# Kernel optimization log

Measured on AMD Instinct MI355X. Metric: run time of the kernel, lower is better.

## Reference

```python
import jax, jax.numpy as jnp
import numpy as np

D_STATE = 16
D_CONV = 4
TOKEN = 8
GROUPS = 4
EPS = 1e-5


def _gn(x, w, b):
    # GroupNorm(GROUPS) over [B,C,H,W]
    B, C, H, W = x.shape
    xr = x.reshape(B, GROUPS, C // GROUPS, H * W)
    mu = xr.mean((2, 3), keepdims=True)
    var = xr.var((2, 3), keepdims=True)
    xn = ((xr - mu) * jax.lax.rsqrt(var + EPS)).reshape(B, C, H, W)
    return xn * w[None, :, None, None] + b[None, :, None, None]


def _mamba(x, in_w, conv_w, conv_b, xp_w, dt_w, dt_b, A_log, Dp, out_w, dt_rank):
    # mamba_ssm Mamba forward: x [B, L, d_model]
    Bn, L, _ = x.shape
    d_inner = conv_w.shape[0]
    xz = jnp.einsum('bld,ed->ble', x, in_w)          # [B,L,2*d_inner]
    xc, z = jnp.split(xz, 2, axis=-1)
    # causal depthwise conv1d (pad left d_conv-1)
    xt = jnp.pad(jnp.transpose(xc, (0, 2, 1)), ((0, 0), (0, 0), (D_CONV - 1, 0)))
    xt = jax.lax.conv_general_dilated(xt, conv_w[:, None, :], (1,), 'VALID',
                                      dimension_numbers=('NCH', 'OIH', 'NCH'),
                                      feature_group_count=d_inner)
    xc = jax.nn.silu(jnp.transpose(xt, (0, 2, 1)) + conv_b)
    dbl = jnp.einsum('ble,fe->blf', xc, xp_w)        # [B,L,dt_rank+2*d_state]
    dt = dbl[..., :dt_rank]
    Bm = dbl[..., dt_rank:dt_rank + D_STATE]
    Cm = dbl[..., dt_rank + D_STATE:]
    delta = jax.nn.softplus(jnp.einsum('blr,er->ble', dt, dt_w) + dt_b)
    A = -jnp.exp(A_log)                              # [d_inner, d_state]

    def step(h, inp):
        u_t, d_t, b_t, c_t = inp                     # [B,d_inner],[B,d_inner],[B,d_state],[B,d_state]
        dA = jnp.exp(d_t[..., None] * A)
        h = h * dA + (d_t * u_t)[..., None] * b_t[:, None, :]
        return h, jnp.sum(h * c_t[:, None, :], axis=-1)

    xs = (jnp.transpose(xc, (1, 0, 2)), jnp.transpose(delta, (1, 0, 2)),
          jnp.transpose(Bm, (1, 0, 2)), jnp.transpose(Cm, (1, 0, 2)))
    h0 = jnp.zeros((Bn, d_inner, D_STATE), x.dtype)
    _, ys = jax.lax.scan(step, h0, xs)
    y = (jnp.transpose(ys, (1, 0, 2)) + xc * Dp) * jax.nn.silu(z)
    return jnp.einsum('ble,de->bld', y, out_w)


def _mamba_params(key, d_model, dt_rank):
    d_inner = 2 * d_model
    ks = jax.random.split(key, 5)
    p = {}
    p['in_w'] = jax.random.normal(ks[0], (2 * d_inner, d_model)) / np.sqrt(d_model).astype(np.float32)
    p['conv_w'] = jax.random.normal(ks[1], (d_inner, D_CONV)) * 0.3
    p['conv_b'] = jnp.zeros((d_inner,))
    p['xp_w'] = jax.random.normal(ks[2], (dt_rank + 2 * D_STATE, d_inner)) / np.sqrt(d_inner).astype(np.float32)
    p['dt_w'] = jax.random.normal(ks[3], (d_inner, dt_rank)) / np.sqrt(dt_rank).astype(np.float32)
    p['dt_b'] = jnp.full((d_inner,), float(np.log(np.expm1(0.01))))
    p['A_log'] = jnp.log(jnp.broadcast_to(jnp.arange(1, D_STATE + 1, dtype=jnp.float32), (d_inner, D_STATE)))
    p['D'] = jnp.ones((d_inner,))
    p['out_w'] = jax.random.normal(ks[4], (d_model, d_inner)) / np.sqrt(d_inner).astype(np.float32)
    return p


def setup_inputs() -> dict:
    key = jax.random.key(0)
    k1, k2, k3 = jax.random.split(key, 3)
    B, C, H, W = 2, 64, 128, 128
    inp = {'x': jax.random.normal(k1, (B, C, H, W), dtype=jnp.float32)}
    spa = _mamba_params(k2, C, 4)
    spe = _mamba_params(k3, C // TOKEN, 1)
    for n, p in (('spa', spa), ('spe', spe)):
        for k, v in p.items():
            inp[f'{n}_{k}'] = v
    inp['spa_gn_w'] = jnp.ones((C,)); inp['spa_gn_b'] = jnp.zeros((C,))
    inp['spe_gn_w'] = jnp.ones((C,)); inp['spe_gn_b'] = jnp.zeros((C,))
    inp['fuse_w'] = jnp.full((2,), 0.5)
    return inp


def reference(x, spa_in_w, spa_conv_w, spa_conv_b, spa_xp_w, spa_dt_w, spa_dt_b,
              spa_A_log, spa_D, spa_out_w, spe_in_w, spe_conv_w, spe_conv_b,
              spe_xp_w, spe_dt_w, spe_dt_b, spe_A_log, spe_D, spe_out_w,
              spa_gn_w, spa_gn_b, spe_gn_w, spe_gn_b, fuse_w):
    B, C, H, W = x.shape
    # SpaMamba: scan over flattened spatial sequence
    xs = jnp.transpose(x, (0, 2, 3, 1)).reshape(B, H * W, C)
    ys = _mamba(xs, spa_in_w, spa_conv_w, spa_conv_b, spa_xp_w, spa_dt_w, spa_dt_b,
                spa_A_log, spa_D, spa_out_w, 4)
    spa = jnp.transpose(ys.reshape(B, H, W, C), (0, 3, 1, 2))
    spa = jax.nn.silu(_gn(spa, spa_gn_w, spa_gn_b)) + x
    # SpeMamba: scan over channel tokens per pixel (C == TOKEN * gc, no padding)
    gc = C // TOKEN
    xe = jnp.transpose(x, (0, 2, 3, 1)).reshape(B * H * W, TOKEN, gc)
    ye = _mamba(xe, spe_in_w, spe_conv_w, spe_conv_b, spe_xp_w, spe_dt_w, spe_dt_b,
                spe_A_log, spe_D, spe_out_w, 1)
    spe = jnp.transpose(ye.reshape(B, H, W, C), (0, 3, 1, 2))
    spe = jax.nn.silu(_gn(spe, spe_gn_w, spe_gn_b)) + x
    w = jax.nn.softmax(fuse_w)
    return spa * w[0] + spe * w[1] + x
```

## Files before the change

kernel.cpp:

```cpp
#include <hip/hip_runtime.h>
#include <math.h>


#define NB 2
#define NC 64
#define HW_ 16384
#define SCH 512
#define SLC 32

__device__ __forceinline__ float sigmoidf_(float v) { return 1.f / (1.f + __expf(-v)); }
__device__ __forceinline__ float siluf_(float v)    { return v * sigmoidf_(v); }
__device__ __forceinline__ float softplusf_(float v) {
    return v > 0.f ? v + log1pf(__expf(-v)) : log1pf(__expf(v));
}

#define K1_XS_OFF 8576
#define K1_XS_STR 68
#define K1_XCL_STR 132

__global__ __launch_bounds__(256) void k1_spatial_pre(
    const float* __restrict__ x, const float* __restrict__ in_w,
    const float* __restrict__ conv_w, const float* __restrict__ conv_b,
    const float* __restrict__ xp_w, const float* __restrict__ dt_w,
    const float* __restrict__ dt_b, const float* __restrict__ A_log,
    float* __restrict__ xc_g, float* __restrict__ sz_g,
    float* __restrict__ dtp_g, float* __restrict__ Bm_g, float* __restrict__ Cm_g,
    float* __restrict__ cumA_g, float* __restrict__ hsum_g)
{
    __shared__ __align__(16) float smem[13132];
    __shared__ __align__(16) float sB[64 * 16];
    __shared__ __align__(16) float sdt[64 * 4];
    const int tid = threadIdx.x;
    const int b   = blockIdx.x >> 8;
    const int l0  = (blockIdx.x & 255) << 6;

    for (int i = tid; i < 67 * 64; i += 256) {
        int c = i / 67;
        int tok = i - c * 67;
        int l = l0 + tok - 3;
        float v = (l >= 0) ? x[((size_t)b * NC + c) * HW_ + l] : 0.f;
        smem[K1_XS_OFF + tok * K1_XS_STR + c] = v;
    }
    __syncthreads();

    {
        const int e = tid & 127;
        const int half = tid >> 7;
        float w[64];
        #pragma unroll
        for (int q = 0; q < 16; ++q) {
            float4 wv = *(const float4*)(in_w + e * 64 + q * 4);
            w[q*4] = wv.x; w[q*4+1] = wv.y; w[q*4+2] = wv.z; w[q*4+3] = wv.w;
        }
        int t0 = half ? 34 : 0, t1 = half ? 67 : 34;
        for (int tok = t0; tok < t1; ++tok) {
            const float4* xr = (const float4*)(smem + K1_XS_OFF + tok * K1_XS_STR);
            float acc = 0.f;
            #pragma unroll
            for (int q = 0; q < 16; ++q) {
                float4 xv = xr[q];
                acc += w[q*4]*xv.x + w[q*4+1]*xv.y + w[q*4+2]*xv.z + w[q*4+3]*xv.w;
            }
            smem[tok * 128 + e] = acc;
        }
        #pragma unroll
        for (int q = 0; q < 16; ++q) {
            float4 wv = *(const float4*)(in_w + (128 + e) * 64 + q * 4);
            w[q*4] = wv.x; w[q*4+1] = wv.y; w[q*4+2] = wv.z; w[q*4+3] = wv.w;
        }
        int z0 = half * 32;
        for (int tok = z0; tok < z0 + 32; ++tok) {
            const float4* xr = (const float4*)(smem + K1_XS_OFF + (tok + 3) * K1_XS_STR);
            float acc = 0.f;
            #pragma unroll
            for (int q = 0; q < 16; ++q) {
                float4 xv = xr[q];
                acc += w[q*4]*xv.x + w[q*4+1]*xv.y + w[q*4+2]*xv.z + w[q*4+3]*xv.w;
            }
            sz_g[((size_t)(b * HW_ + l0 + tok)) * 128 + e] = siluf_(acc);
        }
    }
    __syncthreads();

    {
        const int e = tid & 127;
        float cw0 = conv_w[e*4], cw1 = conv_w[e*4+1], cw2 = conv_w[e*4+2], cw3 = conv_w[e*4+3];
        float cb = conv_b[e];
        float r[32];
        #pragma unroll
        for (int k = 0; k < 32; ++k) {
            int tok = (tid + k * 256) >> 7;
            float v = cb + cw0 * smem[(tok+0)*128 + e] + cw1 * smem[(tok+1)*128 + e]
                         + cw2 * smem[(tok+2)*128 + e] + cw3 * smem[(tok+3)*128 + e];
            v = siluf_(v);
            r[k] = v;
            xc_g[((size_t)(b * HW_ + l0 + tok)) * 128 + e] = v;
        }
        __syncthreads();
        #pragma unroll
        for (int k = 0; k < 32; ++k) {
            int tok = (tid + k * 256) >> 7;
            smem[tok * K1_XCL_STR + e] = r[k];
        }
    }
    __syncthreads();

    for (int i = tid; i < 64 * 32; i += 256) {
        int tok = i >> 5;
        int f = i & 31;
        const float4* xr = (const float4*)(smem + tok * K1_XCL_STR);
        const float4* wr = (const float4*)(xp_w + (4 + f) * 128);
        float acc = 0.f;
        #pragma unroll
        for (int q = 0; q < 32; ++q) {
            float4 a = xr[q], w4 = wr[q];
            acc += a.x*w4.x + a.y*w4.y + a.z*w4.z + a.w*w4.w;
        }
        size_t row = (size_t)(b * HW_ + l0 + tok);
        if (f < 16) { Bm_g[row * 16 + f] = acc; sB[tok * 16 + f] = acc; }
        else        Cm_g[row * 16 + (f - 16)] = acc;
    }
    {
        int tok = tid >> 2;
        const float4* xr = (const float4*)(smem + tok * K1_XCL_STR);
        const float4* wr = (const float4*)(xp_w + (tid & 3) * 128);
        float acc = 0.f;
        #pragma unroll
        for (int q = 0; q < 32; ++q) {
            float4 a = xr[q], w4 = wr[q];
            acc += a.x*w4.x + a.y*w4.y + a.z*w4.z + a.w*w4.w;
        }
        dtp_g[(size_t)(b * HW_ + l0) * 4 + tid] = acc;
        sdt[tid] = acc;
    }
    __syncthreads();

    {
        const int e = tid >> 1;
        const int n0 = (tid & 1) * 8;
        float A[8];
        #pragma unroll
        for (int j = 0; j < 8; ++j) A[j] = -__expf(A_log[e * 16 + n0 + j]);
        float4 wdt = *(const float4*)(dt_w + e * 4);
        float dtb = dt_b[e];
        #pragma unroll 1
        for (int cc = 0; cc < 2; ++cc) {
            float h[8], cA[8];
            #pragma unroll
            for (int j = 0; j < 8; ++j) { h[j] = 0.f; cA[j] = 1.f; }
            for (int t = cc * 32; t < cc * 32 + 32; ++t) {
                float4 dv = *(const float4*)(sdt + t * 4);
                float d = softplusf_(wdt.x*dv.x + wdt.y*dv.y + wdt.z*dv.z + wdt.w*dv.w + dtb);
                float u = smem[t * K1_XCL_STR + e];
                float4 b0 = *(const float4*)(sB + t * 16 + n0);
                float4 b1 = *(const float4*)(sB + t * 16 + n0 + 4);
                float Bv[8]; *(float4*)(Bv) = b0; *(float4*)(Bv + 4) = b1;
                float du = d * u;
                #pragma unroll
                for (int j = 0; j < 8; ++j) {
                    float dA = __expf(d * A[j]);
                    h[j] = h[j] * dA + du * Bv[j];
                    cA[j] *= dA;
                }
            }
            int ch = ((blockIdx.x & 255) << 1) + cc;
            size_t so = ((size_t)b * SCH + ch) * 2048 + tid * 8;
            *(float4*)(cumA_g + so)     = *(float4*)(cA);
            *(float4*)(cumA_g + so + 4) = *(float4*)(cA + 4);
            *(float4*)(hsum_g + so)     = *(float4*)(h);
            *(float4*)(hsum_g + so + 4) = *(float4*)(h + 4);
        }
    }
}

__global__ __launch_bounds__(256) void k3_combine(
    const float* __restrict__ cumA_g, const float* __restrict__ hsum_g,
    float* __restrict__ Hin_g)
{
    int gid = blockIdx.x * 256 + threadIdx.x;
    int b = gid >> 11;
    int en = gid & 2047;
    float st = 0.f;
    size_t o = (size_t)b * SCH * 2048 + en;
    for (int cb = 0; cb < SCH; cb += 16) {
        float a[16], hs[16];
        #pragma unroll
        for (int k = 0; k < 16; ++k) {
            a[k]  = cumA_g[o + (size_t)k * 2048];
            hs[k] = hsum_g[o + (size_t)k * 2048];
        }
        #pragma unroll
        for (int k = 0; k < 16; ++k) {
            Hin_g[o + (size_t)k * 2048] = st;
            st = st * a[k] + hs[k];
        }
        o += (size_t)16 * 2048;
    }
}

__global__ __launch_bounds__(256) void k4_scan2(
    const float* __restrict__ xc_g, const float* __restrict__ sz_g,
    const float* __restrict__ Bm_g, const float* __restrict__ Cm_g,
    const float* __restrict__ dtp_g, const float* __restrict__ dt_w,
    const float* __restrict__ dt_b, const float* __restrict__ A_log,
    const float* __restrict__ Dp, const float* __restrict__ Hin_g,
    const float* __restrict__ out_w,
    float* __restrict__ spa_raw, float* __restrict__ part_spa)
{
    __shared__ __align__(16) float lds[9344];
    float* su  = lds;
    float* sB  = lds + 4096;
    float* sC  = lds + 4608;
    float* sdt = lds + 5120;
    float* yt  = lds + 5248;
    float* ot  = lds;
    __shared__ float wred[32];
    const int tid = threadIdx.x;
    const int b = blockIdx.x >> 9;
    const int ch = blockIdx.x & 511;
    const size_t rowbase = (size_t)b * HW_ + ch * SLC;

    const float4* u4 = (const float4*)(xc_g + rowbase * 128);
    #pragma unroll
    for (int j = 0; j < 4; ++j) ((float4*)su)[tid + j * 256] = u4[tid + j * 256];
    if (tid < 128) ((float4*)sB)[tid] = ((const float4*)(Bm_g + rowbase * 16))[tid];
    else           ((float4*)sC)[tid - 128] = ((const float4*)(Cm_g + rowbase * 16))[tid - 128];
    if (tid < 32)  ((float4*)sdt)[tid] = ((const float4*)(dtp_g + rowbase * 4))[tid];

    const int e = tid >> 1;
    const int nh = tid & 1;
    const int n0 = nh * 8;
    float A[8];
    #pragma unroll
    for (int j = 0; j < 8; ++j) A[j] = -__expf(A_log[e * 16 + n0 + j]);
    float4 wdt = *(const float4*)(dt_w + e * 4);
    float dtb = dt_b[e];
    float Dv = Dp[e];
    float h[8];
    size_t so = (size_t)blockIdx.x * 2048 + tid * 8;
    *(float4*)(h)     = *(const float4*)(Hin_g + so);
    *(float4*)(h + 4) = *(const float4*)(Hin_g + so + 4);
    __syncthreads();

    for (int t = 0; t < SLC; ++t) {
        float4 dv = *(const float4*)(sdt + t * 4);
        float d = softplusf_(wdt.x*dv.x + wdt.y*dv.y + wdt.z*dv.z + wdt.w*dv.w + dtb);
        float u = su[t * 128 + e];
        float4 b0 = *(const float4*)(sB + t * 16 + n0);
        float4 b1 = *(const float4*)(sB + t * 16 + n0 + 4);
        float4 c0 = *(const float4*)(sC + t * 16 + n0);
        float4 c1 = *(const float4*)(sC + t * 16 + n0 + 4);
        float Bv[8]; *(float4*)(Bv) = b0; *(float4*)(Bv + 4) = b1;
        float Cv[8]; *(float4*)(Cv) = c0; *(float4*)(Cv + 4) = c1;
        float du = d * u;
        float y = 0.f;
        #pragma unroll
        for (int j = 0; j < 8; ++j) {
            float dA = __expf(d * A[j]);
            h[j] = h[j] * dA + du * Bv[j];
            y += h[j] * Cv[j];
        }
        y += __shfl_xor(y, 1, 64);
        if (nh == 0) yt[t * 128 + e] = y + u * Dv;
    }
    __syncthreads();

    {
        const float4* sz4 = (const float4*)(sz_g + rowbase * 128);
        #pragma unroll
        for (int j = 0; j < 4; ++j) {
            int f = tid + j * 256;
            float4 yv = ((float4*)yt)[f];
            float4 sv = sz4[f];
            yv.x *= sv.x; yv.y *= sv.y; yv.z *= sv.z; yv.w *= sv.w;
            ((float4*)yt)[f] = yv;
        }
    }
    __syncthreads();

    for (int i = tid; i < 64 * SLC; i += 256) {
        int c = i & 63, t = i >> 6;
        const float4* wr = (const float4*)(out_w + c * 128);
        const float4* yr = (const float4*)(yt + t * 128);
        float acc = 0.f;
        #pragma unroll
        for (int q = 0; q < 32; ++q) {
            float4 w4 = wr[q], yv4 = yr[q];
            acc += w4.x*yv4.x + w4.y*yv4.y + w4.z*yv4.z + w4.w*yv4.w;
        }
        ot[c * 33 + t] = acc;
    }
    __syncthreads();

    for (int i = tid; i < 64 * SLC; i += 256) {
        int c = i >> 5, t = i & 31;
        spa_raw[((size_t)b * NC + c) * HW_ + ch * SLC + t] = ot[c * 33 + t];
    }
    float s[4], s2[4];
    #pragma unroll
    for (int g = 0; g < 4; ++g) {
        float a = 0.f, a2 = 0.f;
        for (int i = tid; i < 512; i += 256) {
            int c = 16 * g + (i >> 5), t = i & 31;
            float v = ot[c * 33 + t];
            a += v; a2 += v * v;
        }
        s[g] = a; s2[g] = a2;
    }
    #pragma unroll
    for (int g = 0; g < 4; ++g) {
        #pragma unroll
        for (int o = 1; o < 64; o <<= 1) {
            s[g]  += __shfl_xor(s[g], o, 64);
            s2[g] += __shfl_xor(s2[g], o, 64);
        }
    }
    if ((tid & 63) == 0) {
        int w = tid >> 6;
        #pragma unroll
        for (int g = 0; g < 4; ++g) { wred[w*8 + g*2] = s[g]; wred[w*8 + g*2 + 1] = s2[g]; }
    }
    __syncthreads();
    if (tid < 8)
        part_spa[tid * 1024 + blockIdx.x] = wred[tid] + wred[8+tid] + wred[16+tid] + wred[24+tid];
}

__global__ __launch_bounds__(256) void k5_spectral(
    const float* __restrict__ x, const float* __restrict__ in_w,
    const float* __restrict__ conv_w, const float* __restrict__ conv_b,
    const float* __restrict__ xp_w, const float* __restrict__ dt_w,
    const float* __restrict__ dt_b, const float* __restrict__ A_log,
    const float* __restrict__ Dp, const float* __restrict__ out_w,
    float* __restrict__ spe_raw, float* __restrict__ part_spe)
{
    __shared__ float xin[16 * 65];
    __shared__ float sBw[16 * 17];
    __shared__ float sCw[16 * 17];
    __shared__ float ys[16 * 136];
    __shared__ float outs[64 * 17];
    __shared__ float wred[32];
    const int tid = threadIdx.x;
    const int b = blockIdx.x >> 10;
    const int hw0 = (blockIdx.x & 1023) << 4;
    const int s = tid >> 4;
    const int l = tid & 15;
    const int base = tid & 48;

    for (int i = tid; i < 1024; i += 256) {
        int c = i >> 4, j = i & 15;
        xin[j * 65 + c] = x[((size_t)b * NC + c) * HW_ + hw0 + j];
    }
    {
        int l2 = tid >> 4, e2 = tid & 15;
        sBw[l2 * 17 + e2] = xp_w[(1 + l2) * 16 + e2];
        sCw[l2 * 17 + e2] = xp_w[(17 + l2) * 16 + e2];
    }

    float wdt[16];
    #pragma unroll
    for (int e = 0; e < 16; ++e) wdt[e] = xp_w[e];
    float wi0[8], wi1[8];
    #pragma unroll
    for (int c = 0; c < 8; ++c) { wi0[c] = in_w[l*8 + c]; wi1[c] = in_w[(l+16)*8 + c]; }
    float cw0 = conv_w[l*4], cw1 = conv_w[l*4+1], cw2 = conv_w[l*4+2], cw3 = conv_w[l*4+3];
    float cb = conv_b[l];
    float dtw = dt_w[l], dtb = dt_b[l];
    __syncthreads();

    float pre[8], sz[8];
    #pragma unroll
    for (int t = 0; t < 8; ++t) {
        float a0 = 0.f, a1 = 0.f;
        #pragma unroll
        for (int c = 0; c < 8; ++c) {
            float xv = xin[s * 65 + t * 8 + c];
            a0 += wi0[c] * xv; a1 += wi1[c] * xv;
        }
        pre[t] = a0; sz[t] = siluf_(a1);
    }
    float xcv[8];
    #pragma unroll
    for (int t = 0; t < 8; ++t) {
        float v = cb + cw3 * pre[t];
        if (t >= 1) v += cw2 * pre[t-1];
        if (t >= 2) v += cw1 * pre[t-2];
        if (t >= 3) v += cw0 * pre[t-3];
        xcv[t] = siluf_(v);
    }

    float bn[8], cn[8], dd0[8];
    #pragma unroll
    for (int t = 0; t < 8; ++t) { bn[t] = 0.f; cn[t] = 0.f; dd0[t] = 0.f; }
    #pragma unroll
    for (int e = 0; e < 16; ++e) {
        float wBe = sBw[l * 17 + e];
        float wCe = sCw[l * 17 + e];
        float wde = wdt[e];
        #pragma unroll
        for (int t = 0; t < 8; ++t) {
            float xv = __shfl(xcv[t], base + e, 64);
            bn[t] += wBe * xv; cn[t] += wCe * xv; dd0[t] += wde * xv;
        }
    }
    float del[8];
    #pragma unroll
    for (int t = 0; t < 8; ++t) del[t] = softplusf_(dd0[t] * dtw + dtb);

    float A[16];
    #pragma unroll
    for (int n = 0; n < 16; ++n) A[n] = -__expf(A_log[l * 16 + n]);
    float Dv = Dp[l];
    float h[16];
    #pragma unroll
    for (int n = 0; n < 16; ++n) h[n] = 0.f;
    #pragma unroll
    for (int t = 0; t < 8; ++t) {
        float d = del[t], u = xcv[t];
        float du = d * u;
        float y = 0.f;
        #pragma unroll
        for (int n = 0; n < 16; ++n) {
            float Bn = __shfl(bn[t], base + n, 64);
            float Cn = __shfl(cn[t], base + n, 64);
            float dA = __expf(d * A[n]);
            h[n] = h[n] * dA + du * Bn;
            y += h[n] * Cn;
        }
        ys[s * 136 + t * 17 + l] = (y + u * Dv) * sz[t];
    }
    __syncthreads();

    {
        int t = l >> 1;
        int db = (l & 1) * 4;
        #pragma unroll
        for (int jj = 0; jj < 4; ++jj) {
            int dd = db + jj;
            float acc = 0.f;
            #pragma unroll
            for (int e = 0; e < 16; ++e) acc += out_w[dd * 16 + e] * ys[s * 136 + t * 17 + e];
            outs[(t * 8 + dd) * 17 + s] = acc;
        }
    }
    __syncthreads();

    float sg[4], sg2[4];
    #pragma unroll
    for (int k = 0; k < 4; ++k) {
        int i = tid + k * 256;
        int c = i >> 4, j = i & 15;
        float v = outs[c * 17 + j];
        spe_raw[((size_t)b * NC + c) * HW_ + hw0 + j] = v;
        sg[k] = v; sg2[k] = v * v;
    }
    #pragma unroll
    for (int k = 0; k < 4; ++k) {
        #pragma unroll
        for (int o = 1; o < 64; o <<= 1) {
            sg[k]  += __shfl_xor(sg[k], o, 64);
            sg2[k] += __shfl_xor(sg2[k], o, 64);
        }
    }
    if ((tid & 63) == 0) {
        int w = tid >> 6;
        #pragma unroll
        for (int k = 0; k < 4; ++k) { wred[w*8 + k*2] = sg[k]; wred[w*8 + k*2 + 1] = sg2[k]; }
    }
    __syncthreads();
    if (tid < 8)
        part_spe[tid * 2048 + blockIdx.x] = wred[tid] + wred[8+tid] + wred[16+tid] + wred[24+tid];
}

__global__ __launch_bounds__(256) void k5b_stats(
    const float* __restrict__ part_spa, const float* __restrict__ part_spe,
    float* __restrict__ stats)
{
    __shared__ float fina[16], fine_[16];
    const int tid = threadIdx.x;
    const int combo = tid >> 4;
    const int ln = tid & 15;
    const int slot = combo & 7, bb = combo >> 3;
    {
        const float4* p = (const float4*)(part_spa + slot * 1024 + bb * 512);
        float a = 0.f;
        #pragma unroll
        for (int k = 0; k < 8; ++k) {
            float4 v = p[ln * 8 + k];
            a += v.x + v.y + v.z + v.w;
        }
        #pragma unroll
        for (int o = 1; o < 16; o <<= 1) a += __shfl_xor(a, o, 64);
        if (ln == 0) fina[combo] = a;
    }
    {
        const float4* p = (const float4*)(part_spe + slot * 2048 + bb * 1024);
        float a = 0.f;
        #pragma unroll
        for (int k = 0; k < 16; ++k) {
            float4 v = p[ln * 16 + k];
            a += v.x + v.y + v.z + v.w;
        }
        #pragma unroll
        for (int o = 1; o < 16; o <<= 1) a += __shfl_xor(a, o, 64);
        if (ln == 0) fine_[combo] = a;
    }
    __syncthreads();
    if (tid < 16) {
        int branch = tid >> 3, bb2 = (tid >> 2) & 1, g = tid & 3;
        const float* fin = branch ? fine_ : fina;
        float S  = fin[bb2 * 8 + g * 2];
        float S2 = fin[bb2 * 8 + g * 2 + 1];
        const float N = 262144.f;
        float mu = S / N;
        float var = S2 / N - mu * mu;
        stats[tid * 2] = mu;
        stats[tid * 2 + 1] = rsqrtf(var + 1e-5f);
    }
}

__global__ __launch_bounds__(256) void k6_fuse(
    const float* __restrict__ x, const float* __restrict__ spa_raw,
    const float* __restrict__ spe_raw, const float* __restrict__ stats,
    const float* __restrict__ gwa, const float* __restrict__ gba,
    const float* __restrict__ gwe, const float* __restrict__ gbe,
    const float* __restrict__ fw, float* __restrict__ out)
{
    size_t i4 = (size_t)blockIdx.x * 256 + threadIdx.x;
    size_t base = i4 * 4;
    int b = (int)(base >> 20);
    int rem = (int)(base & 1048575);
    int c = rem >> 14;
    int g = c >> 4;
    int sidx = (b * 4 + g) * 2;
    float ma = stats[sidx],      ra = stats[sidx + 1];
    float me = stats[16 + sidx], re = stats[16 + sidx + 1];
    float wa = gwa[c], ba = gba[c], we = gwe[c], be = gbe[c];
    float f0 = fw[0], f1 = fw[1];
    float mx = fmaxf(f0, f1);
    float e0 = __expf(f0 - mx), e1 = __expf(f1 - mx);
    float inv = 1.f / (e0 + e1);
    float w0 = e0 * inv, w1 = e1 * inv;
    float4 xv = *(const float4*)(x + base);
    float4 av = *(const float4*)(spa_raw + base);
    float4 ev = *(const float4*)(spe_raw + base);
    float xr[4] = {xv.x, xv.y, xv.z, xv.w};
    float ar[4] = {av.x, av.y, av.z, av.w};
    float er[4] = {ev.x, ev.y, ev.z, ev.w};
    float orr[4];
    #pragma unroll
    for (int k = 0; k < 4; ++k) {
        float spa = siluf_((ar[k] - ma) * ra * wa + ba) + xr[k];
        float spe = siluf_((er[k] - me) * re * we + be) + xr[k];
        orr[k] = spa * w0 + spe * w1 + xr[k];
    }
    float4 ov = {orr[0], orr[1], orr[2], orr[3]};
    *(float4*)(out + base) = ov;
}

extern "C" void kernel_launch(void* const* d_in, const int* in_sizes, int n_in,
                              void* d_out, int out_size, void* d_ws, size_t ws_size,
                              hipStream_t stream)
{
    const float* x      = (const float*)d_in[0];
    const float* a_inw  = (const float*)d_in[1];
    const float* a_cw   = (const float*)d_in[2];
    const float* a_cb   = (const float*)d_in[3];
    const float* a_xp   = (const float*)d_in[4];
    const float* a_dtw  = (const float*)d_in[5];
    const float* a_dtb  = (const float*)d_in[6];
    const float* a_Alog = (const float*)d_in[7];
    const float* a_D    = (const float*)d_in[8];
    const float* a_ow   = (const float*)d_in[9];
    const float* e_inw  = (const float*)d_in[10];
    const float* e_cw   = (const float*)d_in[11];
    const float* e_cb   = (const float*)d_in[12];
    const float* e_xp   = (const float*)d_in[13];
    const float* e_dtw  = (const float*)d_in[14];
    const float* e_dtb  = (const float*)d_in[15];
    const float* e_Alog = (const float*)d_in[16];
    const float* e_D    = (const float*)d_in[17];
    const float* e_ow   = (const float*)d_in[18];
    const float* gwa    = (const float*)d_in[19];
    const float* gba    = (const float*)d_in[20];
    const float* gwe    = (const float*)d_in[21];
    const float* gbe    = (const float*)d_in[22];
    const float* fw     = (const float*)d_in[23];

    float* ws    = (float*)d_ws;
    float* xc    = ws;
    float* sz    = xc    + 4194304;
    float* Bm    = sz    + 4194304;
    float* Cm    = Bm    + 524288;
    float* dtp   = Cm    + 524288;
    float* cumA  = dtp   + 131072;
    float* hsum  = cumA  + 2097152;
    float* Hin   = hsum  + 2097152;
    float* spa_r = Hin   + 2097152;
    float* spe_r = spa_r + 2097152;
    float* pspa  = spe_r + 2097152;
    float* pspe  = pspa  + 8192;
    float* stats = pspe  + 16384;

    k1_spatial_pre<<<512, 256, 0, stream>>>(x, a_inw, a_cw, a_cb, a_xp, a_dtw,
                                            a_dtb, a_Alog,
                                            xc, sz, dtp, Bm, Cm, cumA, hsum);
    k3_combine<<<16, 256, 0, stream>>>(cumA, hsum, Hin);
    k5_spectral<<<2048, 256, 0, stream>>>(x, e_inw, e_cw, e_cb, e_xp, e_dtw, e_dtb,
                                          e_Alog, e_D, e_ow, spe_r, pspe);
    k4_scan2<<<1024, 256, 0, stream>>>(xc, sz, Bm, Cm, dtp, a_dtw, a_dtb, a_Alog,
                                       a_D, Hin, a_ow, spa_r, pspa);
    k5b_stats<<<1, 256, 0, stream>>>(pspa, pspe, stats);
    k6_fuse<<<2048, 256, 0, stream>>>(x, spa_r, spe_r, stats, gwa, gba, gwe, gbe, fw,
                                      (float*)d_out);
}
```

Before: 413.6 us.

## Halve spatial pre-kernel tile and restage spectral B/C projections through LDS

```diff
diff --git a/kernel.cpp b/kernel.cpp
--- a/kernel.cpp
+++ b/kernel.cpp
@@ -14,7 +14,7 @@
     return v > 0.f ? v + log1pf(__expf(-v)) : log1pf(__expf(v));
 }
 
-#define K1_XS_OFF 8576
+#define K1_XS_OFF 4480
 #define K1_XS_STR 68
 #define K1_XCL_STR 132
 
@@ -27,16 +27,16 @@
     float* __restrict__ dtp_g, float* __restrict__ Bm_g, float* __restrict__ Cm_g,
     float* __restrict__ cumA_g, float* __restrict__ hsum_g)
 {
-    __shared__ __align__(16) float smem[13132];
-    __shared__ __align__(16) float sB[64 * 16];
-    __shared__ __align__(16) float sdt[64 * 4];
+    __shared__ __align__(16) float smem[6860];
+    __shared__ __align__(16) float sB[32 * 16];
+    __shared__ __align__(16) float sdt[32 * 4];
     const int tid = threadIdx.x;
-    const int b   = blockIdx.x >> 8;
-    const int l0  = (blockIdx.x & 255) << 6;
-
-    for (int i = tid; i < 67 * 64; i += 256) {
-        int c = i / 67;
-        int tok = i - c * 67;
+    const int b   = blockIdx.x >> 9;
+    const int l0  = (blockIdx.x & 511) << 5;
+
+    for (int i = tid; i < 35 * 64; i += 256) {
+        int c = i / 35;
+        int tok = i - c * 35;
         int l = l0 + tok - 3;
         float v = (l >= 0) ? x[((size_t)b * NC + c) * HW_ + l] : 0.f;
         smem[K1_XS_OFF + tok * K1_XS_STR + c] = v;
@@ -52,7 +52,7 @@
             float4 wv = *(const float4*)(in_w + e * 64 + q * 4);
             w[q*4] = wv.x; w[q*4+1] = wv.y; w[q*4+2] = wv.z; w[q*4+3] = wv.w;
         }
-        int t0 = half ? 34 : 0, t1 = half ? 67 : 34;
+        int t0 = half ? 18 : 0, t1 = half ? 35 : 18;
         for (int tok = t0; tok < t1; ++tok) {
             const float4* xr = (const float4*)(smem + K1_XS_OFF + tok * K1_XS_STR);
             float acc = 0.f;
@@ -68,8 +68,8 @@
             float4 wv = *(const float4*)(in_w + (128 + e) * 64 + q * 4);
             w[q*4] = wv.x; w[q*4+1] = wv.y; w[q*4+2] = wv.z; w[q*4+3] = wv.w;
         }
-        int z0 = half * 32;
-        for (int tok = z0; tok < z0 + 32; ++tok) {
+        int z0 = half * 16;
+        for (int tok = z0; tok < z0 + 16; ++tok) {
             const float4* xr = (const float4*)(smem + K1_XS_OFF + (tok + 3) * K1_XS_STR);
             float acc = 0.f;
             #pragma unroll
@@ -86,9 +86,9 @@
         const int e = tid & 127;
         float cw0 = conv_w[e*4], cw1 = conv_w[e*4+1], cw2 = conv_w[e*4+2], cw3 = conv_w[e*4+3];
         float cb = conv_b[e];
-        float r[32];
-        #pragma unroll
-        for (int k = 0; k < 32; ++k) {
+        float r[16];
+        #pragma unroll
+        for (int k = 0; k < 16; ++k) {
             int tok = (tid + k * 256) >> 7;
             float v = cb + cw0 * smem[(tok+0)*128 + e] + cw1 * smem[(tok+1)*128 + e]
                          + cw2 * smem[(tok+2)*128 + e] + cw3 * smem[(tok+3)*128 + e];
@@ -98,14 +98,14 @@
         }
         __syncthreads();
         #pragma unroll
-        for (int k = 0; k < 32; ++k) {
+        for (int k = 0; k < 16; ++k) {
             int tok = (tid + k * 256) >> 7;
             smem[tok * K1_XCL_STR + e] = r[k];
         }
     }
     __syncthreads();
 
-    for (int i = tid; i < 64 * 32; i += 256) {
+    for (int i = tid; i < 32 * 32; i += 256) {
         int tok = i >> 5;
         int f = i & 31;
         const float4* xr = (const float4*)(smem + tok * K1_XCL_STR);
@@ -120,7 +120,7 @@
         if (f < 16) { Bm_g[row * 16 + f] = acc; sB[tok * 16 + f] = acc; }
         else        Cm_g[row * 16 + (f - 16)] = acc;
     }
-    {
+    if (tid < 128) {
         int tok = tid >> 2;
         const float4* xr = (const float4*)(smem + tok * K1_XCL_STR);
         const float4* wr = (const float4*)(xp_w + (tid & 3) * 128);
@@ -143,33 +143,29 @@
         for (int j = 0; j < 8; ++j) A[j] = -__expf(A_log[e * 16 + n0 + j]);
         float4 wdt = *(const float4*)(dt_w + e * 4);
         float dtb = dt_b[e];
-        #pragma unroll 1
-        for (int cc = 0; cc < 2; ++cc) {
-            float h[8], cA[8];
+        float h[8], cA[8];
+        #pragma unroll
+        for (int j = 0; j < 8; ++j) { h[j] = 0.f; cA[j] = 1.f; }
+        for (int t = 0; t < 32; ++t) {
+            float4 dv = *(const float4*)(sdt + t * 4);
+            float d = softplusf_(wdt.x*dv.x + wdt.y*dv.y + wdt.z*dv.z + wdt.w*dv.w + dtb);
+            float u = smem[t * K1_XCL_STR + e];
+            float4 b0 = *(const float4*)(sB + t * 16 + n0);
+            float4 b1 = *(const float4*)(sB + t * 16 + n0 + 4);
+            float Bv[8]; *(float4*)(Bv) = b0; *(float4*)(Bv + 4) = b1;
+            float du = d * u;
             #pragma unroll
-            for (int j = 0; j < 8; ++j) { h[j] = 0.f; cA[j] = 1.f; }
-            for (int t = cc * 32; t < cc * 32 + 32; ++t) {
-                float4 dv = *(const float4*)(sdt + t * 4);
-                float d = softplusf_(wdt.x*dv.x + wdt.y*dv.y + wdt.z*dv.z + wdt.w*dv.w + dtb);
-                float u = smem[t * K1_XCL_STR + e];
-                float4 b0 = *(const float4*)(sB + t * 16 + n0);
-                float4 b1 = *(const float4*)(sB + t * 16 + n0 + 4);
-                float Bv[8]; *(float4*)(Bv) = b0; *(float4*)(Bv + 4) = b1;
-                float du = d * u;
-                #pragma unroll
-                for (int j = 0; j < 8; ++j) {
-                    float dA = __expf(d * A[j]);
-                    h[j] = h[j] * dA + du * Bv[j];
-                    cA[j] *= dA;
-                }
+            for (int j = 0; j < 8; ++j) {
+                float dA = __expf(d * A[j]);
+                h[j] = h[j] * dA + du * Bv[j];
+                cA[j] *= dA;
             }
-            int ch = ((blockIdx.x & 255) << 1) + cc;
-            size_t so = ((size_t)b * SCH + ch) * 2048 + tid * 8;
-            *(float4*)(cumA_g + so)     = *(float4*)(cA);
-            *(float4*)(cumA_g + so + 4) = *(float4*)(cA + 4);
-            *(float4*)(hsum_g + so)     = *(float4*)(h);
-            *(float4*)(hsum_g + so + 4) = *(float4*)(h + 4);
-        }
+        }
+        size_t so = (size_t)blockIdx.x * 2048 + tid * 8;
+        *(float4*)(cumA_g + so)     = *(float4*)(cA);
+        *(float4*)(cumA_g + so + 4) = *(float4*)(cA + 4);
+        *(float4*)(hsum_g + so)     = *(float4*)(h);
+        *(float4*)(hsum_g + so + 4) = *(float4*)(h + 4);
     }
 }
 
@@ -325,7 +321,9 @@
         part_spa[tid * 1024 + blockIdx.x] = wred[tid] + wred[8+tid] + wred[16+tid] + wred[24+tid];
 }
 
-__global__ __launch_bounds__(256) void k5_spectral(
+#define K5_STR 144
+
+__global__ __launch_bounds__(256, 2) void k5_spectral(
     const float* __restrict__ x, const float* __restrict__ in_w,
     const float* __restrict__ conv_w, const float* __restrict__ conv_b,
     const float* __restrict__ xp_w, const float* __restrict__ dt_w,
@@ -333,49 +331,50 @@
     const float* __restrict__ Dp, const float* __restrict__ out_w,
     float* __restrict__ spe_raw, float* __restrict__ part_spe)
 {
-    __shared__ float xin[16 * 65];
-    __shared__ float sBw[16 * 17];
-    __shared__ float sCw[16 * 17];
-    __shared__ float ys[16 * 136];
-    __shared__ float outs[64 * 17];
+    __shared__ __align__(16) float lds[7936];
+    float* xcs  = lds;
+    float* sBn  = lds + 2304;
+    float* sCn  = lds + 4608;
+    float* souw = lds + 6912;
+    float* xin  = sBn;
+    float* ys   = xcs;
+    float* outs = sCn;
     __shared__ float wred[32];
     const int tid = threadIdx.x;
     const int b = blockIdx.x >> 10;
     const int hw0 = (blockIdx.x & 1023) << 4;
     const int s = tid >> 4;
     const int l = tid & 15;
-    const int base = tid & 48;
 
     for (int i = tid; i < 1024; i += 256) {
         int c = i >> 4, j = i & 15;
-        xin[j * 65 + c] = x[((size_t)b * NC + c) * HW_ + hw0 + j];
-    }
-    {
-        int l2 = tid >> 4, e2 = tid & 15;
-        sBw[l2 * 17 + e2] = xp_w[(1 + l2) * 16 + e2];
-        sCw[l2 * 17 + e2] = xp_w[(17 + l2) * 16 + e2];
-    }
-
-    float wdt[16];
-    #pragma unroll
-    for (int e = 0; e < 16; ++e) wdt[e] = xp_w[e];
+        xin[j * 68 + c] = x[((size_t)b * NC + c) * HW_ + hw0 + j];
+        souw[i] = out_w[i];
+    }
     float wi0[8], wi1[8];
     #pragma unroll
     for (int c = 0; c < 8; ++c) { wi0[c] = in_w[l*8 + c]; wi1[c] = in_w[(l+16)*8 + c]; }
     float cw0 = conv_w[l*4], cw1 = conv_w[l*4+1], cw2 = conv_w[l*4+2], cw3 = conv_w[l*4+3];
     float cb = conv_b[l];
     float dtw = dt_w[l], dtb = dt_b[l];
+    float wdt[16], wB[16], wC[16];
+    #pragma unroll
+    for (int e = 0; e < 16; ++e) {
+        wdt[e] = xp_w[e];
+        wB[e]  = xp_w[(1 + l) * 16 + e];
+        wC[e]  = xp_w[(17 + l) * 16 + e];
+    }
     __syncthreads();
 
     float pre[8], sz[8];
     #pragma unroll
     for (int t = 0; t < 8; ++t) {
-        float a0 = 0.f, a1 = 0.f;
-        #pragma unroll
-        for (int c = 0; c < 8; ++c) {
-            float xv = xin[s * 65 + t * 8 + c];
-            a0 += wi0[c] * xv; a1 += wi1[c] * xv;
-        }
+        float4 x0 = *(const float4*)(xin + s * 68 + t * 8);
+        float4 x1 = *(const float4*)(xin + s * 68 + t * 8 + 4);
+        float a0 = wi0[0]*x0.x + wi0[1]*x0.y + wi0[2]*x0.z + wi0[3]*x0.w
+                 + wi0[4]*x1.x + wi0[5]*x1.y + wi0[6]*x1.z + wi0[7]*x1.w;
+        float a1 = wi1[0]*x0.x + wi1[1]*x0.y + wi1[2]*x0.z + wi1[3]*x0.w
+                 + wi1[4]*x1.x + wi1[5]*x1.y + wi1[6]*x1.z + wi1[7]*x1.w;
         pre[t] = a0; sz[t] = siluf_(a1);
     }
     float xcv[8];
@@ -387,24 +386,32 @@
         if (t >= 3) v += cw0 * pre[t-3];
         xcv[t] = siluf_(v);
     }
-
-    float bn[8], cn[8], dd0[8];
-    #pragma unroll
-    for (int t = 0; t < 8; ++t) { bn[t] = 0.f; cn[t] = 0.f; dd0[t] = 0.f; }
-    #pragma unroll
-    for (int e = 0; e < 16; ++e) {
-        float wBe = sBw[l * 17 + e];
-        float wCe = sCw[l * 17 + e];
-        float wde = wdt[e];
-        #pragma unroll
-        for (int t = 0; t < 8; ++t) {
-            float xv = __shfl(xcv[t], base + e, 64);
-            bn[t] += wBe * xv; cn[t] += wCe * xv; dd0[t] += wde * xv;
-        }
-    }
+    #pragma unroll
+    for (int t = 0; t < 8; ++t) xcs[s * K5_STR + t * 16 + l] = xcv[t];
+    __syncthreads();
+
     float del[8];
     #pragma unroll
-    for (int t = 0; t < 8; ++t) del[t] = softplusf_(dd0[t] * dtw + dtb);
+    for (int t = 0; t < 8; ++t) {
+        const float4* xr = (const float4*)(xcs + s * K5_STR + t * 16);
+        float4 v0 = xr[0], v1 = xr[1], v2 = xr[2], v3 = xr[3];
+        float bn = wB[0]*v0.x + wB[1]*v0.y + wB[2]*v0.z + wB[3]*v0.w
+                 + wB[4]*v1.x + wB[5]*v1.y + wB[6]*v1.z + wB[7]*v1.w
+                 + wB[8]*v2.x + wB[9]*v2.y + wB[10]*v2.z + wB[11]*v2.w
+                 + wB[12]*v3.x + wB[13]*v3.y + wB[14]*v3.z + wB[15]*v3.w;
+        float cn = wC[0]*v0.x + wC[1]*v0.y + wC[2]*v0.z + wC[3]*v0.w
+                 + wC[4]*v1.x + wC[5]*v1.y + wC[6]*v1.z + wC[7]*v1.w
+                 + wC[8]*v2.x + wC[9]*v2.y + wC[10]*v2.z + wC[11]*v2.w
+                 + wC[12]*v3.x + wC[13]*v3.y + wC[14]*v3.z + wC[15]*v3.w;
+        float d0 = wdt[0]*v0.x + wdt[1]*v0.y + wdt[2]*v0.z + wdt[3]*v0.w
+                 + wdt[4]*v1.x + wdt[5]*v1.y + wdt[6]*v1.z + wdt[7]*v1.w
+                 + wdt[8]*v2.x + wdt[9]*v2.y + wdt[10]*v2.z + wdt[11]*v2.w
+                 + wdt[12]*v3.x + wdt[13]*v3.y + wdt[14]*v3.z + wdt[15]*v3.w;
+        sBn[s * K5_STR + t * 16 + l] = bn;
+        sCn[s * K5_STR + t * 16 + l] = cn;
+        del[t] = softplusf_(d0 * dtw + dtb);
+    }
+    __syncthreads();
 
     float A[16];
     #pragma unroll
@@ -418,27 +425,35 @@
         float d = del[t], u = xcv[t];
         float du = d * u;
         float y = 0.f;
-        #pragma unroll
-        for (int n = 0; n < 16; ++n) {
-            float Bn = __shfl(bn[t], base + n, 64);
-            float Cn = __shfl(cn[t], base + n, 64);
-            float dA = __expf(d * A[n]);
-            h[n] = h[n] * dA + du * Bn;
-            y += h[n] * Cn;
-        }
-        ys[s * 136 + t * 17 + l] = (y + u * Dv) * sz[t];
+        const float4* Bp = (const float4*)(sBn + s * K5_STR + t * 16);
+        const float4* Cp = (const float4*)(sCn + s * K5_STR + t * 16);
+        #pragma unroll
+        for (int q = 0; q < 4; ++q) {
+            float4 Bq = Bp[q], Cq = Cp[q];
+            float dA;
+            dA = __expf(d*A[4*q+0]); h[4*q+0] = h[4*q+0]*dA + du*Bq.x; y += h[4*q+0]*Cq.x;
+            dA = __expf(d*A[4*q+1]); h[4*q+1] = h[4*q+1]*dA + du*Bq.y; y += h[4*q+1]*Cq.y;
+            dA = __expf(d*A[4*q+2]); h[4*q+2] = h[4*q+2]*dA + du*Bq.z; y += h[4*q+2]*Cq.z;
+            dA = __expf(d*A[4*q+3]); h[4*q+3] = h[4*q+3]*dA + du*Bq.w; y += h[4*q+3]*Cq.w;
+        }
+        ys[s * K5_STR + t * 16 + l] = (y + u * Dv) * sz[t];
     }
     __syncthreads();
 
     {
         int t = l >> 1;
         int db = (l & 1) * 4;
+        const float4* yr = (const float4*)(ys + s * K5_STR + t * 16);
+        float4 y0 = yr[0], y1 = yr[1], y2 = yr[2], y3 = yr[3];
         #pragma unroll
         for (int jj = 0; jj < 4; ++jj) {
             int dd = db + jj;
-            float acc = 0.f;
-            #pragma unroll
-            for (int e = 0; e < 16; ++e) acc += out_w[dd * 16 + e] * ys[s * 136 + t * 17 + e];
+            const float4* wr = (const float4*)(souw + dd * 16);
+            float4 w0 = wr[0], w1 = wr[1], w2 = wr[2], w3 = wr[3];
+            float acc = w0.x*y0.x + w0.y*y0.y + w0.z*y0.z + w0.w*y0.w
+                      + w1.x*y1.x + w1.y*y1.y + w1.z*y1.z + w1.w*y1.w
+                      + w2.x*y2.x + w2.y*y2.y + w2.z*y2.z + w2.w*y2.w
+                      + w3.x*y3.x + w3.y*y3.y + w3.z*y3.z + w3.w*y3.w;
             outs[(t * 8 + dd) * 17 + s] = acc;
         }
     }
@@ -601,9 +616,9 @@
     float* pspe  = pspa  + 8192;
     float* stats = pspe  + 16384;
 
-    k1_spatial_pre<<<512, 256, 0, stream>>>(x, a_inw, a_cw, a_cb, a_xp, a_dtw,
-                                            a_dtb, a_Alog,
-                                            xc, sz, dtp, Bm, Cm, cumA, hsum);
+    k1_spatial_pre<<<1024, 256, 0, stream>>>(x, a_inw, a_cw, a_cb, a_xp, a_dtw,
+                                             a_dtb, a_Alog,
+                                             xc, sz, dtp, Bm, Cm, cumA, hsum);
     k3_combine<<<16, 256, 0, stream>>>(cumA, hsum, Hin);
     k5_spectral<<<2048, 256, 0, stream>>>(x, e_inw, e_cw, e_cb, e_xp, e_dtw, e_dtb,
                                           e_Alog, e_D, e_ow, spe_r, pspe);
```

After: 361.2 us. 12.7% less time.
